# Kernel optimization log

Measured on AMD Instinct MI355X. Metric: run time of the kernel, lower is better.

The kernel has to match this reference:

```python
import jax, jax.numpy as jnp
import numpy as np

B, N, NH, H = 32, 512, 4, 32      # batch, agents per group, heads, hidden per head
IN_DIM, OUT_DIM = 128, 128
BIG = 9.0e15
SQRT_DK = float(np.sqrt(H))


def setup_inputs() -> dict:
    key = jax.random.key(0)
    keys = iter(jax.random.split(key, 64))

    def nrm(shape, scale=0.05):
        return jax.random.normal(next(keys), shape, dtype=jnp.float32) * scale

    inp = {}
    inp["x0"] = jax.random.normal(next(keys), (B, N, IN_DIM), dtype=jnp.float32)
    inp["x1"] = jax.random.normal(next(keys), (B, N, IN_DIM), dtype=jnp.float32)
    for name in ("m00", "m01", "m10", "m11"):
        inp[name] = jax.random.randint(next(keys), (B, N, N), 0, 2, dtype=jnp.int32)
    # per-group q/k/v projections: Linear(in_dim, NH*H)
    for g in (0, 1):
        inp[f"wq{g}"] = nrm((IN_DIM, NH * H)); inp[f"bq{g}"] = nrm((NH * H,))
        inp[f"wk{g}"] = nrm((IN_DIM, NH * H)); inp[f"bk{g}"] = nrm((NH * H,))
        inp[f"wv{g}"] = nrm((IN_DIM, NH * H)); inp[f"bv{g}"] = nrm((NH * H,))
    # fc_outs[i][j]: Linear(NH*H, H)
    for i in (0, 1):
        for j in (0, 1):
            inp[f"wo{i}{j}"] = nrm((NH * H, H)); inp[f"bo{i}{j}"] = nrm((H,))
    # fc_out_final[i]: Linear(H * 2, out_dim)
    for g in (0, 1):
        inp[f"wf{g}"] = nrm((2 * H, OUT_DIM)); inp[f"bf{g}"] = nrm((OUT_DIM,))
    return inp


def _qkv(x, wq, bq, wk, bk, wv, bv):
    q = jax.nn.relu(x @ wq + bq)
    k = jax.nn.relu(x @ wk + bk)
    v = jax.nn.relu(x @ wv + bv)
    return q, k, v


def _split_heads(t):
    # [B, N, NH*H] -> [B, NH, N, H]; contiguous H-blocks == torch per-head slices
    return t.reshape(B, t.shape[1], NH, H).transpose(0, 2, 1, 3)


def _attend(q, k, v, mask, gate):
    qh, kh, vh = _split_heads(q), _split_heads(k), _split_heads(v)
    logits = jnp.einsum('bhqd,bhkd->bhqk', qh, kh) / SQRT_DK
    m = mask.astype(logits.dtype)[:, None]            # [B,1,Nq,Nk]
    w = jax.nn.softmax(logits * m - BIG * (1.0 - m), axis=-1)
    if gate:
        has = (mask.sum(axis=-1) > 0).astype(w.dtype)  # [B,Nq]
        w = w * has[:, None, :, None]
    out = jnp.einsum('bhqk,bhkd->bhqd', w, vh)
    # heads concatenated along feature dim (matches torch.cat of head slices)
    return out.transpose(0, 2, 1, 3).reshape(B, q.shape[1], NH * H)


def reference(x0, x1, m00, m01, m10, m11,
              wq0, bq0, wk0, bk0, wv0, bv0,
              wq1, bq1, wk1, bk1, wv1, bv1,
              wo00, bo00, wo01, bo01, wo10, bo10, wo11, bo11,
              wf0, bf0, wf1, bf1):
    q0, k0, v0 = _qkv(x0, wq0, bq0, wk0, bk0, wv0, bv0)
    q1, k1, v1 = _qkv(x1, wq1, bq1, wk1, bk1, wv1, bv1)
    inner0 = jax.nn.relu(_attend(q0, k0, v0, m00, gate=False) @ wo00 + bo00)
    inner1 = jax.nn.relu(_attend(q1, k1, v1, m11, gate=False) @ wo11 + bo11)
    inter0 = jax.nn.relu(_attend(q0, k1, v1, m01, gate=True) @ wo01 + bo01)
    inter1 = jax.nn.relu(_attend(q1, k0, v0, m10, gate=True) @ wo10 + bo10)
    out0 = jnp.concatenate([inner0, inter0], axis=-1) @ wf0 + bf0
    out1 = jnp.concatenate([inner1, inter1], axis=-1) @ wf1 + bf1
    return (out0, out1)
```

## Files before the change

### kernel.cpp

```cpp
#include <hip/hip_runtime.h>

#define B_    32
#define N_    512
#define D_    128
#define ROWS  (B_ * N_)
#define SCALE2_ (0.17677669529663687f * 1.4426950408889634f)

typedef __bf16 bf16x8 __attribute__((ext_vector_type(8)));
typedef __bf16 bf16x4 __attribute__((ext_vector_type(4)));
typedef float  f32x4  __attribute__((ext_vector_type(4)));

static __device__ __forceinline__ f32x4 mfma16(bf16x8 a, bf16x8 b, f32x4 c) {
  return __builtin_amdgcn_mfma_f32_16x16x32_bf16(a, b, c, 0, 0, 0);
}

__global__ __launch_bounds__(256) void prep_kernel(
    const int* __restrict__ m00, const int* __restrict__ m01,
    const int* __restrict__ m10, const int* __restrict__ m11,
    const float* __restrict__ wq0, const float* __restrict__ wk0, const float* __restrict__ wv0,
    const float* __restrict__ wq1, const float* __restrict__ wk1, const float* __restrict__ wv1,
    const float* __restrict__ wo00, const float* __restrict__ wo01,
    const float* __restrict__ wo10, const float* __restrict__ wo11,
    const float* __restrict__ wf0, const float* __restrict__ wf1,
    __bf16* __restrict__ wtb, __bf16* __restrict__ wob, __bf16* __restrict__ wfb,
    unsigned long long* __restrict__ mpk)
{
  const int bx = blockIdx.x, t = threadIdx.x;
  if (bx < 16384) {
    const int wid = bx * 4 + (t >> 6);
    const int lane = t & 63;
    const int row = wid & 511, b = (wid >> 9) & 31, a = wid >> 14;
    const int* msel = (a == 0) ? m00 : (a == 1) ? m11 : (a == 2) ? m01 : m10;
    const int* src = msel + ((size_t)b * N_ + row) * N_;
    unsigned long long mine = 0;
    #pragma unroll
    for (int ch = 0; ch < 8; ++ch) {
      const int v = src[ch * 64 + lane];
      const unsigned long long bits = __ballot(v != 0);
      if (lane == ch) mine = bits;
    }
    if (lane < 8)
      mpk[((size_t)(a * 32 + b) * 8 + lane) * 512 + row] = mine;
  } else if (bx < 16480) {
    const int i = bx - 16384, mat = i >> 4, sub = i & 15;
    const float* w = (mat == 0) ? wq0 : (mat == 1) ? wk0 : (mat == 2) ? wv0
                   : (mat == 3) ? wq1 : (mat == 4) ? wk1 : wv1;
    __bf16* dst = wtb + mat * 16384;
    const int fidx = sub * 256 + t;
    const float4 f = ((const float4*)w)[fidx];
    const int e = fidx * 4, k = e >> 7, n = e & 127;
    dst[(n + 0) * 128 + k] = (__bf16)f.x;
    dst[(n + 1) * 128 + k] = (__bf16)f.y;
    dst[(n + 2) * 128 + k] = (__bf16)f.z;
    dst[(n + 3) * 128 + k] = (__bf16)f.w;
  } else if (bx < 16496) {
    const int i = bx - 16480, a = i >> 2, sub = i & 3;
    const float* w = (a == 0) ? wo00 : (a == 1) ? wo11 : (a == 2) ? wo01 : wo10;
    __bf16* dst = wob + a * 4096;
    const int fidx = sub * 256 + t;
    const float4 f = ((const float4*)w)[fidx];
    const int e = fidx * 4, k = e >> 5, n = e & 31;
    dst[(n + 0) * 128 + k] = (__bf16)f.x;
    dst[(n + 1) * 128 + k] = (__bf16)f.y;
    dst[(n + 2) * 128 + k] = (__bf16)f.z;
    dst[(n + 3) * 128 + k] = (__bf16)f.w;
  } else {
    const int i = bx - 16496, g = i >> 3, sub = i & 7;
    const float* w = g ? wf1 : wf0;
    __bf16* dst = wfb + g * 8192;
    const int d0 = sub * 1024 + t * 4;
    const int n = d0 >> 6, k = d0 & 63;
    bf16x4 v;
    #pragma unroll
    for (int j = 0; j < 4; ++j) v[j] = (__bf16)w[(size_t)(k + j) * 128 + n];
    *(bf16x4*)&dst[d0] = v;
  }
}

__global__ __launch_bounds__(256) void qkv_kernel(
    const float* __restrict__ x0, const float* __restrict__ x1,
    const float* __restrict__ bq0, const float* __restrict__ bk0, const float* __restrict__ bv0,
    const float* __restrict__ bq1, const float* __restrict__ bk1, const float* __restrict__ bv1,
    const __bf16* __restrict__ wtb, __bf16* __restrict__ qkvb)
{
  __shared__ __align__(16) __bf16 vtile[128][72];
  const int bx = blockIdx.x;
  const int g = bx >> 8, tile = bx & 255, R0 = tile * 64;
  const int t = threadIdx.x, lane = t & 63, wave = t >> 6;
  const int quad = lane >> 4, ln = lane & 15;
  const float* xs = g ? x1 : x0;

  bf16x8 af[4];
  {
    const int row = R0 + wave * 16 + ln;
    #pragma unroll
    for (int ks = 0; ks < 4; ++ks) {
      const float4* xp = (const float4*)(xs + (size_t)row * D_ + ks * 32 + quad * 8);
      float4 a = xp[0], b = xp[1];
      bf16x8 v;
      v[0] = (__bf16)a.x; v[1] = (__bf16)a.y; v[2] = (__bf16)a.z; v[3] = (__bf16)a.w;
      v[4] = (__bf16)b.x; v[5] = (__bf16)b.y; v[6] = (__bf16)b.z; v[7] = (__bf16)b.w;
      af[ks] = v;
    }
  }
  const f32x4 zero4 = {0.f, 0.f, 0.f, 0.f};

  for (int m = 0; m < 3; ++m) {
    const __bf16* wt = wtb + (g * 3 + m) * 16384;
    const float* bias = (g == 0) ? ((m == 0) ? bq0 : (m == 1) ? bk0 : bv0)
                                 : ((m == 0) ? bq1 : (m == 1) ? bk1 : bv1);
    __bf16* outp = qkvb + (size_t)(g * 3 + m) * (ROWS * D_);

    f32x4 acc[8];
    #pragma unroll
    for (int nt = 0; nt < 8; ++nt) acc[nt] = zero4;
    #pragma unroll
    for (int ks = 0; ks < 4; ++ks) {
      #pragma unroll
      for (int nt = 0; nt < 8; ++nt) {
        bf16x8 bfrag = *(const bf16x8*)(wt + (size_t)(nt * 16 + ln) * D_ + ks * 32 + quad * 8);
        acc[nt] = mfma16(af[ks], bfrag, acc[nt]);
      }
    }

    if (m != 2) {
      const float sc = (m == 0) ? SCALE2_ : 1.0f;
      #pragma unroll
      for (int nt = 0; nt < 8; ++nt) {
        const int col = nt * 16 + ln;
        const float bv = bias[col];
        #pragma unroll
        for (int r = 0; r < 4; ++r) {
          float v = fmaxf(acc[nt][r] + bv, 0.f) * sc;
          outp[(size_t)(R0 + wave * 16 + quad * 4 + r) * D_ + col] = (__bf16)v;
        }
      }
    } else {
      #pragma unroll
      for (int nt = 0; nt < 8; ++nt) {
        const int col = nt * 16 + ln;
        const float bv = bias[col];
        #pragma unroll
        for (int r = 0; r < 4; ++r) {
          float v = fmaxf(acc[nt][r] + bv, 0.f);
          vtile[col][wave * 16 + quad * 4 + r] = (__bf16)v;
        }
      }
      __syncthreads();
      const int b = R0 >> 9, kb2 = R0 & 511;
      const int dim = t >> 1, off = (t & 1) * 32;
      uint4* dst = (uint4*)(outp + (size_t)b * (D_ * N_) + (size_t)dim * N_ + kb2 + off);
      const uint4* srcp = (const uint4*)&vtile[dim][off];
      #pragma unroll
      for (int i = 0; i < 4; ++i) dst[i] = srcp[i];
    }
  }
}

__global__ __launch_bounds__(256, 2) void attn_kernel(
    const __bf16* __restrict__ qkvb,
    const unsigned long long* __restrict__ mpk,
    const __bf16* __restrict__ wob,
    const float* __restrict__ bo00, const float* __restrict__ bo01,
    const float* __restrict__ bo10, const float* __restrict__ bo11,
    __bf16* __restrict__ projb)
{
  __shared__ __align__(16) __bf16 raw[16384];

  const int bx = blockIdx.x;
  const int qt = bx >> 7, cb = bx & 127, a = cb >> 5, b = cb & 31;
  const int t = threadIdx.x, lane = t & 63, h = t >> 6;
  const int quad = lane >> 4, ln = lane & 15;

  const int qg = (a == 1 || a == 3) ? 1 : 0;
  const int kg = (a == 1 || a == 2) ? 1 : 0;
  const float* bo = (a == 0) ? bo00 : (a == 1) ? bo11 : (a == 2) ? bo01 : bo10;

  const __bf16* qb  = qkvb + (size_t)(qg * 3 + 0) * (ROWS * D_) + (size_t)(b * N_ + qt * 64) * D_;
  const __bf16* kb  = qkvb + (size_t)(kg * 3 + 1) * (ROWS * D_) + (size_t)b * N_ * D_;
  const __bf16* vtb = qkvb + (size_t)(kg * 3 + 2) * (ROWS * D_) + (size_t)b * D_ * N_;
  const unsigned long long* mrow = mpk + (size_t)(a * 32 + b) * 8 * 512 + qt * 64;

  __bf16* PT = raw + h * 4096;

  bf16x8 qf[4];
  #pragma unroll
  for (int bt = 0; bt < 4; ++bt)
    qf[bt] = *(const bf16x8*)(qb + (size_t)(bt * 16 + ln) * D_ + h * 32 + quad * 8);

  const f32x4 zero4 = {0.f, 0.f, 0.f, 0.f};
  f32x4 Oacc[2][4];
  float lp[4];
  #pragma unroll
  for (int bt = 0; bt < 4; ++bt) {
    lp[bt] = 0.f;
    Oacc[0][bt] = zero4; Oacc[1][bt] = zero4;
  }

  unsigned long long mb[4];
  #pragma unroll
  for (int bt = 0; bt < 4; ++bt) mb[bt] = mrow[bt * 16 + ln];

  for (int ch = 0; ch < 8; ++ch) {
    const int kc = ch * 64;

    unsigned long long mbn[4] = {0, 0, 0, 0};
    if (ch < 7) {
      #pragma unroll
      for (int bt = 0; bt < 4; ++bt)
        mbn[bt] = mrow[(size_t)(ch + 1) * 512 + bt * 16 + ln];
    }

    #pragma unroll
    for (int at = 0; at < 4; ++at) {
      bf16x8 kf = *(const bf16x8*)(kb + (size_t)(kc + at * 16 + ln) * D_ + h * 32 + quad * 8);
      #pragma unroll
      for (int bt = 0; bt < 4; ++bt) {
        f32x4 s = mfma16(kf, qf[bt], zero4);
        bf16x4 pv;
        float ps = 0.f;
        #pragma unroll
        for (int r = 0; r < 4; ++r) {
          const int bit = (int)((mb[bt] >> (at * 16 + quad * 4 + r)) & 1ull);
          const float p = bit ? __builtin_amdgcn_exp2f(s[r]) : 0.f;
          ps += p;
          pv[r] = (__bf16)p;
        }
        lp[bt] += ps;
        const int row = bt * 16 + ln;
        const int blk = (2 * at + (quad >> 1)) ^ (ln & 7);
        *(bf16x4*)&PT[row * 64 + blk * 8 + (quad & 1) * 4] = pv;
      }
    }

    #pragma unroll
    for (int s2 = 0; s2 < 2; ++s2) {
      bf16x8 pb[4];
      #pragma unroll
      for (int bt = 0; bt < 4; ++bt) {
        const int row = bt * 16 + ln;
        const int blk = (4 * s2 + quad) ^ (ln & 7);
        pb[bt] = *(const bf16x8*)&PT[row * 64 + blk * 8];
      }
      #pragma unroll
      for (int d = 0; d < 2; ++d) {
        bf16x8 vf = *(const bf16x8*)(vtb + (size_t)(h * 32 + d * 16 + ln) * N_ + kc + s2 * 32 + quad * 8);
        #pragma unroll
        for (int bt = 0; bt < 4; ++bt)
          Oacc[d][bt] = mfma16(vf, pb[bt], Oacc[d][bt]);
      }
    }

    #pragma unroll
    for (int bt = 0; bt < 4; ++bt) mb[bt] = mbn[bt];
  }

  float fac[4];
  #pragma unroll
  for (int bt = 0; bt < 4; ++bt) {
    float l = lp[bt] + __shfl_xor(lp[bt], 16);
    l += __shfl_xor(l, 32);
    fac[bt] = (l > 0.f) ? 1.f / l : 0.f;
  }

  __syncthreads();
  __bf16* OL = raw;
  #pragma unroll
  for (int d = 0; d < 2; ++d)
    #pragma unroll
    for (int bt = 0; bt < 4; ++bt) {
      bf16x4 ov;
      #pragma unroll
      for (int r = 0; r < 4; ++r) ov[r] = (__bf16)(Oacc[d][bt][r] * fac[bt]);
      *(bf16x4*)&OL[(bt * 16 + ln) * 136 + h * 32 + d * 16 + quad * 4] = ov;
    }
  __syncthreads();

  const __bf16* wo = wob + a * 4096;
  f32x4 pacc[2];
  pacc[0] = zero4; pacc[1] = zero4;
  #pragma unroll
  for (int ks = 0; ks < 4; ++ks) {
    bf16x8 afr = *(const bf16x8*)&OL[(h * 16 + ln) * 136 + ks * 32 + quad * 8];
    #pragma unroll
    for (int ct = 0; ct < 2; ++ct) {
      bf16x8 bw = *(const bf16x8*)(wo + (size_t)(ct * 16 + ln) * D_ + ks * 32 + quad * 8);
      pacc[ct] = mfma16(afr, bw, pacc[ct]);
    }
  }
  const int R0g = b * N_ + qt * 64;
  #pragma unroll
  for (int ct = 0; ct < 2; ++ct) {
    const int col = ct * 16 + ln;
    const float bv = bo[col];
    #pragma unroll
    for (int r = 0; r < 4; ++r) {
      const float v = fmaxf(pacc[ct][r] + bv, 0.f);
      projb[(size_t)(a * ROWS + R0g + h * 16 + quad * 4 + r) * 32 + col] = (__bf16)v;
    }
  }
}

__global__ __launch_bounds__(256) void outproj_kernel(
    const __bf16* __restrict__ projb, const __bf16* __restrict__ wfb,
    const float* __restrict__ bf0, const float* __restrict__ bf1,
    float* __restrict__ out)
{
  const int t = threadIdx.x, lane = t & 63, w = t >> 6;
  const int quad = lane >> 4, ln = lane & 15;
  const int row = blockIdx.x * 64 + w * 16;
  const f32x4 zero4 = {0.f, 0.f, 0.f, 0.f};

  #pragma unroll
  for (int g = 0; g < 2; ++g) {
    const float* bfp = g ? bf1 : bf0;
    f32x4 acc[8];
    #pragma unroll
    for (int ct = 0; ct < 8; ++ct) acc[ct] = zero4;
    #pragma unroll
    for (int s = 0; s < 2; ++s) {
      const int asrc = s ? (2 + g) : g;
      bf16x8 afr = *(const bf16x8*)(projb + (size_t)(asrc * ROWS + row + ln) * 32 + quad * 8);
      const __bf16* wb = wfb + g * 8192 + s * 32;
      #pragma unroll
      for (int ct = 0; ct < 8; ++ct) {
        bf16x8 bw = *(const bf16x8*)(wb + (size_t)(ct * 16 + ln) * 64 + quad * 8);
        acc[ct] = mfma16(afr, bw, acc[ct]);
      }
    }
    float* og = out + (size_t)g * (ROWS * D_);
    #pragma unroll
    for (int ct = 0; ct < 8; ++ct) {
      const int col = ct * 16 + ln;
      const float bv = bfp[col];
      #pragma unroll
      for (int r = 0; r < 4; ++r)
        og[(size_t)(row + quad * 4 + r) * D_ + col] = acc[ct][r] + bv;
    }
  }
}

extern "C" void kernel_launch(void* const* d_in, const int* in_sizes, int n_in,
                              void* d_out, int out_size, void* d_ws, size_t ws_size,
                              hipStream_t stream)
{
  const float* x0 = (const float*)d_in[0];
  const float* x1 = (const float*)d_in[1];
  const int* m00 = (const int*)d_in[2];
  const int* m01 = (const int*)d_in[3];
  const int* m10 = (const int*)d_in[4];
  const int* m11 = (const int*)d_in[5];
  const float* wq0 = (const float*)d_in[6];  const float* bq0 = (const float*)d_in[7];
  const float* wk0 = (const float*)d_in[8];  const float* bk0 = (const float*)d_in[9];
  const float* wv0 = (const float*)d_in[10]; const float* bv0 = (const float*)d_in[11];
  const float* wq1 = (const float*)d_in[12]; const float* bq1 = (const float*)d_in[13];
  const float* wk1 = (const float*)d_in[14]; const float* bk1 = (const float*)d_in[15];
  const float* wv1 = (const float*)d_in[16]; const float* bv1 = (const float*)d_in[17];
  const float* wo00 = (const float*)d_in[18]; const float* bo00 = (const float*)d_in[19];
  const float* wo01 = (const float*)d_in[20]; const float* bo01 = (const float*)d_in[21];
  const float* wo10 = (const float*)d_in[22]; const float* bo10 = (const float*)d_in[23];
  const float* wo11 = (const float*)d_in[24]; const float* bo11 = (const float*)d_in[25];
  const float* wf0 = (const float*)d_in[26]; const float* bf0 = (const float*)d_in[27];
  const float* wf1 = (const float*)d_in[28]; const float* bf1 = (const float*)d_in[29];

  __bf16* qkvb = (__bf16*)d_ws;
  __bf16* projb = (__bf16*)((char*)d_ws + 25165824);
  __bf16* wtb  = (__bf16*)((char*)d_ws + 29360128);
  __bf16* wob  = (__bf16*)((char*)d_ws + 29556736);
  __bf16* wfb  = (__bf16*)((char*)d_ws + 29589504);
  unsigned long long* mpk = (unsigned long long*)((char*)d_ws + 29622272);

  prep_kernel<<<dim3(16512), dim3(256), 0, stream>>>(
      m00, m01, m10, m11, wq0, wk0, wv0, wq1, wk1, wv1,
      wo00, wo01, wo10, wo11, wf0, wf1, wtb, wob, wfb, mpk);
  qkv_kernel<<<dim3(512), dim3(256), 0, stream>>>(
      x0, x1, bq0, bk0, bv0, bq1, bk1, bv1, wtb, qkvb);
  attn_kernel<<<dim3(1024), dim3(256), 0, stream>>>(
      qkvb, mpk, wob, bo00, bo01, bo10, bo11, projb);
  outproj_kernel<<<dim3(256), dim3(256), 0, stream>>>(
      projb, wfb, bf0, bf1, (float*)d_out);
}
```

Before: 302.3 us.

## Split attention over key halves with a combine kernel and widen qkv/outproj grids

Attention is split into two key-range halves per query tile, doubling the grid. Each half writes unnormalized partial outputs and row sums to workspace, and a new combine kernel sums them, normalizes, and applies the per-pair projection. The qkv and output-projection kernels now give each matrix or group its own block instead of looping inside one block, so more blocks run in parallel. The cost is an extra kernel launch and a round trip of the partial outputs through global memory, and the next-chunk mask prefetch is dropped.

```diff
diff --git a/kernel.cpp b/kernel.cpp
--- a/kernel.cpp
+++ b/kernel.cpp
@@ -85,10 +85,15 @@
 {
   __shared__ __align__(16) __bf16 vtile[128][72];
   const int bx = blockIdx.x;
-  const int g = bx >> 8, tile = bx & 255, R0 = tile * 64;
+  const int mat = bx >> 8, tile = bx & 255, R0 = tile * 64;
+  const int m = mat % 3;
   const int t = threadIdx.x, lane = t & 63, wave = t >> 6;
   const int quad = lane >> 4, ln = lane & 15;
-  const float* xs = g ? x1 : x0;
+  const float* xs = (mat < 3) ? x0 : x1;
+  const float* bias = (mat == 0) ? bq0 : (mat == 1) ? bk0 : (mat == 2) ? bv0
+                    : (mat == 3) ? bq1 : (mat == 4) ? bk1 : bv1;
+  const __bf16* wt = wtb + mat * 16384;
+  __bf16* outp = qkvb + (size_t)mat * (ROWS * D_);
 
   bf16x8 af[4];
   {
@@ -105,76 +110,66 @@
   }
   const f32x4 zero4 = {0.f, 0.f, 0.f, 0.f};
 
-  for (int m = 0; m < 3; ++m) {
-    const __bf16* wt = wtb + (g * 3 + m) * 16384;
-    const float* bias = (g == 0) ? ((m == 0) ? bq0 : (m == 1) ? bk0 : bv0)
-                                 : ((m == 0) ? bq1 : (m == 1) ? bk1 : bv1);
-    __bf16* outp = qkvb + (size_t)(g * 3 + m) * (ROWS * D_);
-
-    f32x4 acc[8];
-    #pragma unroll
-    for (int nt = 0; nt < 8; ++nt) acc[nt] = zero4;
-    #pragma unroll
-    for (int ks = 0; ks < 4; ++ks) {
-      #pragma unroll
-      for (int nt = 0; nt < 8; ++nt) {
-        bf16x8 bfrag = *(const bf16x8*)(wt + (size_t)(nt * 16 + ln) * D_ + ks * 32 + quad * 8);
-        acc[nt] = mfma16(af[ks], bfrag, acc[nt]);
-      }
-    }
-
-    if (m != 2) {
-      const float sc = (m == 0) ? SCALE2_ : 1.0f;
-      #pragma unroll
-      for (int nt = 0; nt < 8; ++nt) {
-        const int col = nt * 16 + ln;
-        const float bv = bias[col];
-        #pragma unroll
-        for (int r = 0; r < 4; ++r) {
-          float v = fmaxf(acc[nt][r] + bv, 0.f) * sc;
-          outp[(size_t)(R0 + wave * 16 + quad * 4 + r) * D_ + col] = (__bf16)v;
-        }
-      }
-    } else {
-      #pragma unroll
-      for (int nt = 0; nt < 8; ++nt) {
-        const int col = nt * 16 + ln;
-        const float bv = bias[col];
-        #pragma unroll
-        for (int r = 0; r < 4; ++r) {
-          float v = fmaxf(acc[nt][r] + bv, 0.f);
-          vtile[col][wave * 16 + quad * 4 + r] = (__bf16)v;
-        }
-      }
-      __syncthreads();
-      const int b = R0 >> 9, kb2 = R0 & 511;
-      const int dim = t >> 1, off = (t & 1) * 32;
-      uint4* dst = (uint4*)(outp + (size_t)b * (D_ * N_) + (size_t)dim * N_ + kb2 + off);
-      const uint4* srcp = (const uint4*)&vtile[dim][off];
-      #pragma unroll
-      for (int i = 0; i < 4; ++i) dst[i] = srcp[i];
-    }
+  f32x4 acc[8];
+  #pragma unroll
+  for (int nt = 0; nt < 8; ++nt) acc[nt] = zero4;
+  #pragma unroll
+  for (int ks = 0; ks < 4; ++ks) {
+    #pragma unroll
+    for (int nt = 0; nt < 8; ++nt) {
+      bf16x8 bfrag = *(const bf16x8*)(wt + (size_t)(nt * 16 + ln) * D_ + ks * 32 + quad * 8);
+      acc[nt] = mfma16(af[ks], bfrag, acc[nt]);
+    }
+  }
+
+  if (m != 2) {
+    const float sc = (m == 0) ? SCALE2_ : 1.0f;
+    #pragma unroll
+    for (int nt = 0; nt < 8; ++nt) {
+      const int col = nt * 16 + ln;
+      const float bv = bias[col];
+      #pragma unroll
+      for (int r = 0; r < 4; ++r) {
+        float v = fmaxf(acc[nt][r] + bv, 0.f) * sc;
+        outp[(size_t)(R0 + wave * 16 + quad * 4 + r) * D_ + col] = (__bf16)v;
+      }
+    }
+  } else {
+    #pragma unroll
+    for (int nt = 0; nt < 8; ++nt) {
+      const int col = nt * 16 + ln;
+      const float bv = bias[col];
+      #pragma unroll
+      for (int r = 0; r < 4; ++r) {
+        float v = fmaxf(acc[nt][r] + bv, 0.f);
+        vtile[col][wave * 16 + quad * 4 + r] = (__bf16)v;
+      }
+    }
+    __syncthreads();
+    const int b = R0 >> 9, kb2 = R0 & 511;
+    const int dim = t >> 1, off = (t & 1) * 32;
+    uint4* dst = (uint4*)(outp + (size_t)b * (D_ * N_) + (size_t)dim * N_ + kb2 + off);
+    const uint4* srcp = (const uint4*)&vtile[dim][off];
+    #pragma unroll
+    for (int i = 0; i < 4; ++i) dst[i] = srcp[i];
   }
 }
 
 __global__ __launch_bounds__(256, 2) void attn_kernel(
     const __bf16* __restrict__ qkvb,
     const unsigned long long* __restrict__ mpk,
-    const __bf16* __restrict__ wob,
-    const float* __restrict__ bo00, const float* __restrict__ bo01,
-    const float* __restrict__ bo10, const float* __restrict__ bo11,
-    __bf16* __restrict__ projb)
+    __bf16* __restrict__ Opart,
+    float* __restrict__ lpart)
 {
   __shared__ __align__(16) __bf16 raw[16384];
 
   const int bx = blockIdx.x;
-  const int qt = bx >> 7, cb = bx & 127, a = cb >> 5, b = cb & 31;
+  const int half = bx >> 10, qt = (bx >> 7) & 7, cb = bx & 127, a = cb >> 5, b = cb & 31;
   const int t = threadIdx.x, lane = t & 63, h = t >> 6;
   const int quad = lane >> 4, ln = lane & 15;
 
   const int qg = (a == 1 || a == 3) ? 1 : 0;
   const int kg = (a == 1 || a == 2) ? 1 : 0;
-  const float* bo = (a == 0) ? bo00 : (a == 1) ? bo11 : (a == 2) ? bo01 : bo10;
 
   const __bf16* qb  = qkvb + (size_t)(qg * 3 + 0) * (ROWS * D_) + (size_t)(b * N_ + qt * 64) * D_;
   const __bf16* kb  = qkvb + (size_t)(kg * 3 + 1) * (ROWS * D_) + (size_t)b * N_ * D_;
@@ -197,19 +192,13 @@
     Oacc[0][bt] = zero4; Oacc[1][bt] = zero4;
   }
 
-  unsigned long long mb[4];
-  #pragma unroll
-  for (int bt = 0; bt < 4; ++bt) mb[bt] = mrow[bt * 16 + ln];
-
-  for (int ch = 0; ch < 8; ++ch) {
+  for (int ch = half * 4; ch < half * 4 + 4; ++ch) {
     const int kc = ch * 64;
 
-    unsigned long long mbn[4] = {0, 0, 0, 0};
-    if (ch < 7) {
-      #pragma unroll
-      for (int bt = 0; bt < 4; ++bt)
-        mbn[bt] = mrow[(size_t)(ch + 1) * 512 + bt * 16 + ln];
-    }
+    unsigned long long mb[4];
+    #pragma unroll
+    for (int bt = 0; bt < 4; ++bt)
+      mb[bt] = mrow[(size_t)ch * 512 + bt * 16 + ln];
 
     #pragma unroll
     for (int at = 0; at < 4; ++at) {
@@ -250,45 +239,69 @@
           Oacc[d][bt] = mfma16(vf, pb[bt], Oacc[d][bt]);
       }
     }
-
-    #pragma unroll
-    for (int bt = 0; bt < 4; ++bt) mb[bt] = mbn[bt];
-  }
-
-  float fac[4];
+  }
+
+  const int R0g = b * N_ + qt * 64;
+  const size_t obase = (size_t)half * 4 * ROWS + (size_t)a * ROWS + R0g;
   #pragma unroll
   for (int bt = 0; bt < 4; ++bt) {
     float l = lp[bt] + __shfl_xor(lp[bt], 16);
     l += __shfl_xor(l, 32);
-    fac[bt] = (l > 0.f) ? 1.f / l : 0.f;
-  }
-
-  __syncthreads();
-  __bf16* OL = raw;
+    if (quad == 0) lpart[(obase + bt * 16 + ln) * 4 + h] = l;
+  }
   #pragma unroll
   for (int d = 0; d < 2; ++d)
     #pragma unroll
     for (int bt = 0; bt < 4; ++bt) {
       bf16x4 ov;
       #pragma unroll
-      for (int r = 0; r < 4; ++r) ov[r] = (__bf16)(Oacc[d][bt][r] * fac[bt]);
-      *(bf16x4*)&OL[(bt * 16 + ln) * 136 + h * 32 + d * 16 + quad * 4] = ov;
-    }
-  __syncthreads();
+      for (int r = 0; r < 4; ++r) ov[r] = (__bf16)Oacc[d][bt][r];
+      *(bf16x4*)&Opart[(obase + bt * 16 + ln) * 128 + h * 32 + d * 16 + quad * 4] = ov;
+    }
+}
+
+__global__ __launch_bounds__(256) void combine_kernel(
+    const __bf16* __restrict__ Opart, const float* __restrict__ lpart,
+    const __bf16* __restrict__ wob,
+    const float* __restrict__ bo00, const float* __restrict__ bo01,
+    const float* __restrict__ bo10, const float* __restrict__ bo11,
+    __bf16* __restrict__ projb)
+{
+  const int bx = blockIdx.x;
+  const int qt = bx >> 7, cb = bx & 127, a = cb >> 5, b = cb & 31;
+  const int t = threadIdx.x, lane = t & 63, h = t >> 6;
+  const int quad = lane >> 4, ln = lane & 15;
+  const float* bo = (a == 0) ? bo00 : (a == 1) ? bo11 : (a == 2) ? bo01 : bo10;
+
+  const int R0g = b * N_ + qt * 64;
+  const size_t idx = (size_t)a * ROWS + R0g + h * 16 + ln;
+
+  const float4 l1 = *(const float4*)&lpart[idx * 4];
+  const float4 l2 = *(const float4*)&lpart[((size_t)4 * ROWS + idx) * 4];
+  float fac[4];
+  fac[0] = (l1.x + l2.x > 0.f) ? 1.f / (l1.x + l2.x) : 0.f;
+  fac[1] = (l1.y + l2.y > 0.f) ? 1.f / (l1.y + l2.y) : 0.f;
+  fac[2] = (l1.z + l2.z > 0.f) ? 1.f / (l1.z + l2.z) : 0.f;
+  fac[3] = (l1.w + l2.w > 0.f) ? 1.f / (l1.w + l2.w) : 0.f;
 
   const __bf16* wo = wob + a * 4096;
+  const f32x4 zero4 = {0.f, 0.f, 0.f, 0.f};
   f32x4 pacc[2];
   pacc[0] = zero4; pacc[1] = zero4;
   #pragma unroll
   for (int ks = 0; ks < 4; ++ks) {
-    bf16x8 afr = *(const bf16x8*)&OL[(h * 16 + ln) * 136 + ks * 32 + quad * 8];
+    bf16x8 o1 = *(const bf16x8*)&Opart[idx * 128 + ks * 32 + quad * 8];
+    bf16x8 o2 = *(const bf16x8*)&Opart[((size_t)4 * ROWS + idx) * 128 + ks * 32 + quad * 8];
+    bf16x8 af;
+    #pragma unroll
+    for (int j = 0; j < 8; ++j)
+      af[j] = (__bf16)(((float)o1[j] + (float)o2[j]) * fac[ks]);
     #pragma unroll
     for (int ct = 0; ct < 2; ++ct) {
       bf16x8 bw = *(const bf16x8*)(wo + (size_t)(ct * 16 + ln) * D_ + ks * 32 + quad * 8);
-      pacc[ct] = mfma16(afr, bw, pacc[ct]);
-    }
-  }
-  const int R0g = b * N_ + qt * 64;
+      pacc[ct] = mfma16(af, bw, pacc[ct]);
+    }
+  }
   #pragma unroll
   for (int ct = 0; ct < 2; ++ct) {
     const int col = ct * 16 + ln;
@@ -306,37 +319,36 @@
     const float* __restrict__ bf0, const float* __restrict__ bf1,
     float* __restrict__ out)
 {
+  const int bx = blockIdx.x;
+  const int g = bx >> 8, tile = bx & 255;
   const int t = threadIdx.x, lane = t & 63, w = t >> 6;
   const int quad = lane >> 4, ln = lane & 15;
-  const int row = blockIdx.x * 64 + w * 16;
+  const int row = tile * 64 + w * 16;
   const f32x4 zero4 = {0.f, 0.f, 0.f, 0.f};
 
-  #pragma unroll
-  for (int g = 0; g < 2; ++g) {
-    const float* bfp = g ? bf1 : bf0;
-    f32x4 acc[8];
-    #pragma unroll
-    for (int ct = 0; ct < 8; ++ct) acc[ct] = zero4;
-    #pragma unroll
-    for (int s = 0; s < 2; ++s) {
-      const int asrc = s ? (2 + g) : g;
-      bf16x8 afr = *(const bf16x8*)(projb + (size_t)(asrc * ROWS + row + ln) * 32 + quad * 8);
-      const __bf16* wb = wfb + g * 8192 + s * 32;
-      #pragma unroll
-      for (int ct = 0; ct < 8; ++ct) {
-        bf16x8 bw = *(const bf16x8*)(wb + (size_t)(ct * 16 + ln) * 64 + quad * 8);
-        acc[ct] = mfma16(afr, bw, acc[ct]);
-      }
-    }
-    float* og = out + (size_t)g * (ROWS * D_);
+  const float* bfp = g ? bf1 : bf0;
+  f32x4 acc[8];
+  #pragma unroll
+  for (int ct = 0; ct < 8; ++ct) acc[ct] = zero4;
+  #pragma unroll
+  for (int s = 0; s < 2; ++s) {
+    const int asrc = s ? (2 + g) : g;
+    bf16x8 afr = *(const bf16x8*)(projb + (size_t)(asrc * ROWS + row + ln) * 32 + quad * 8);
+    const __bf16* wb = wfb + g * 8192 + s * 32;
     #pragma unroll
     for (int ct = 0; ct < 8; ++ct) {
-      const int col = ct * 16 + ln;
-      const float bv = bfp[col];
-      #pragma unroll
-      for (int r = 0; r < 4; ++r)
-        og[(size_t)(row + quad * 4 + r) * D_ + col] = acc[ct][r] + bv;
-    }
+      bf16x8 bw = *(const bf16x8*)(wb + (size_t)(ct * 16 + ln) * 64 + quad * 8);
+      acc[ct] = mfma16(afr, bw, acc[ct]);
+    }
+  }
+  float* og = out + (size_t)g * (ROWS * D_);
+  #pragma unroll
+  for (int ct = 0; ct < 8; ++ct) {
+    const int col = ct * 16 + ln;
+    const float bv = bfp[col];
+    #pragma unroll
+    for (int r = 0; r < 4; ++r)
+      og[(size_t)(row + quad * 4 + r) * D_ + col] = acc[ct][r] + bv;
   }
 }
 
@@ -369,14 +381,18 @@
   __bf16* wob  = (__bf16*)((char*)d_ws + 29556736);
   __bf16* wfb  = (__bf16*)((char*)d_ws + 29589504);
   unsigned long long* mpk = (unsigned long long*)((char*)d_ws + 29622272);
+  __bf16* Opart = (__bf16*)((char*)d_ws + 33816576);
+  float* lpart  = (float*)((char*)d_ws + 67371008);
 
   prep_kernel<<<dim3(16512), dim3(256), 0, stream>>>(
       m00, m01, m10, m11, wq0, wk0, wv0, wq1, wk1, wv1,
       wo00, wo01, wo10, wo11, wf0, wf1, wtb, wob, wfb, mpk);
-  qkv_kernel<<<dim3(512), dim3(256), 0, stream>>>(
+  qkv_kernel<<<dim3(1536), dim3(256), 0, stream>>>(
       x0, x1, bq0, bk0, bv0, bq1, bk1, bv1, wtb, qkvb);
-  attn_kernel<<<dim3(1024), dim3(256), 0, stream>>>(
-      qkvb, mpk, wob, bo00, bo01, bo10, bo11, projb);
-  outproj_kernel<<<dim3(256), dim3(256), 0, stream>>>(
+  attn_kernel<<<dim3(2048), dim3(256), 0, stream>>>(
+      qkvb, mpk, Opart, lpart);
+  combine_kernel<<<dim3(1024), dim3(256), 0, stream>>>(
+      Opart, lpart, wob, bo00, bo01, bo10, bo11, projb);
+  outproj_kernel<<<dim3(512), dim3(256), 0, stream>>>(
       projb, wfb, bf0, bf1, (float*)d_out);
 }
```

Result: slower. 322.5 us (+6.7%).
